# Optimization experiments

Measured on AMD Instinct MI355X. Metric: run time of the kernel, lower is better.

The kernel has to match this reference:

```python
import jax, jax.numpy as jnp
import numpy as np

N_NODES = 50000
N_EDGES = 800000
IN_FEATS = 256
HIDDEN = 128
OUT_FEATS = 64


def setup_inputs() -> dict:
    key = jax.random.key(0)
    k1, k2, k3, k4, k5 = jax.random.split(key, 5)
    x = jax.random.normal(k1, (N_NODES, IN_FEATS), dtype=jnp.float32)
    src = jax.random.randint(k2, (N_EDGES,), 0, N_NODES, dtype=jnp.int64)
    dst = jax.random.randint(k3, (N_EDGES,), 0, N_NODES, dtype=jnp.int64)
    # Glorot-ish init for linear weights (DGL GraphConv uses xavier_uniform)
    W1 = jax.random.normal(k4, (IN_FEATS, HIDDEN), dtype=jnp.float32) / np.sqrt(IN_FEATS)
    W2 = jax.random.normal(k5, (HIDDEN, OUT_FEATS), dtype=jnp.float32) / np.sqrt(HIDDEN)
    b1 = jnp.zeros((HIDDEN,), dtype=jnp.float32)
    b2 = jnp.zeros((OUT_FEATS,), dtype=jnp.float32)
    return {"x": x, "src": src, "dst": dst, "W1": W1, "b1": b1, "W2": W2, "b2": b2}


def _norms(src, dst, n_nodes):
    ones = jnp.ones(src.shape[0], dtype=jnp.float32)
    deg_out = jax.ops.segment_sum(ones, src, num_segments=n_nodes)
    deg_in = jax.ops.segment_sum(ones, dst, num_segments=n_nodes)
    # DGL clamps zero degrees to 1 to avoid inf
    norm_src = jnp.power(jnp.clip(deg_out, 1.0, None), -0.5)  # [N]
    norm_dst = jnp.power(jnp.clip(deg_in, 1.0, None), -0.5)   # [N]
    return norm_src, norm_dst


def _gcn_layer(h, W, b, src, dst, norm_src, norm_dst, n_nodes):
    # norm='both': D_dst^{-1/2} A D_src^{-1/2} (h W) + b
    # multiply by W first (in_feats >= out_feats -> cheaper aggregation)
    m = (h * norm_src[:, None]) @ W            # [N, out]
    agg = jax.ops.segment_sum(m[src], dst, num_segments=n_nodes)  # [N, out]
    return agg * norm_dst[:, None] + b


def reference(x, src, dst, W1, b1, W2, b2):
    n = x.shape[0]
    norm_src, norm_dst = _norms(src, dst, n)
    h = _gcn_layer(x, W1, b1, src, dst, norm_src, norm_dst, n)
    h = jax.nn.relu(h)
    h = _gcn_layer(h, W2, b2, src, dst, norm_src, norm_dst, n)
    return h
```

## Files before the change

### kernel.cpp

```cpp
#include <hip/hip_runtime.h>

#define N_NODES 50000
#define N_EDGES 800000
#define IN_FEATS 256
#define HIDDEN 128
#define OUT_FEATS 64

#define NB 8192
#define NRANGE 7
#define NBT (NRANGE * NB)
#define NCHUNK 64
#define EPC 12500

typedef _Float16 f16;
typedef _Float16 f16x2 __attribute__((ext_vector_type(2)));
typedef _Float16 f16x8 __attribute__((ext_vector_type(8)));
typedef float f32x4 __attribute__((ext_vector_type(4)));

__global__ __launch_bounds__(256) void hist_kernel(
    const int* __restrict__ src, const int* __restrict__ dst,
    int* __restrict__ hist_src, int* __restrict__ hist_dst) {
  __shared__ int ls[NB];
  __shared__ int ld2[NB];
  const int r = blockIdx.x % NRANGE;
  const int c = blockIdx.x / NRANGE;
  const int lo = r * NB;
  for (int i = threadIdx.x; i < NB; i += 256) {
    ls[i] = 0;
    ld2[i] = 0;
  }
  __syncthreads();
  const int4* s4 = (const int4*)(src + c * EPC);
  const int4* d4 = (const int4*)(dst + c * EPC);
  for (int i = threadIdx.x; i < EPC / 4; i += 256) {
    int4 s = s4[i];
    int4 d = d4[i];
    unsigned b;
    b = (unsigned)(s.x - lo); if (b < NB) atomicAdd(&ls[b], 1);
    b = (unsigned)(s.y - lo); if (b < NB) atomicAdd(&ls[b], 1);
    b = (unsigned)(s.z - lo); if (b < NB) atomicAdd(&ls[b], 1);
    b = (unsigned)(s.w - lo); if (b < NB) atomicAdd(&ls[b], 1);
    b = (unsigned)(d.x - lo); if (b < NB) atomicAdd(&ld2[b], 1);
    b = (unsigned)(d.y - lo); if (b < NB) atomicAdd(&ld2[b], 1);
    b = (unsigned)(d.z - lo); if (b < NB) atomicAdd(&ld2[b], 1);
    b = (unsigned)(d.w - lo); if (b < NB) atomicAdd(&ld2[b], 1);
  }
  __syncthreads();
  int* hs = hist_src + (long)c * NBT + lo;
  int* hd = hist_dst + (long)c * NBT + lo;
  for (int i = threadIdx.x; i < NB; i += 256) {
    hs[i] = ls[i];
    hd[i] = ld2[i];
  }
}

__global__ __launch_bounds__(256) void reduce_kernel(
    const int* __restrict__ hist_src, int* __restrict__ hist_dst,
    int* __restrict__ deg_in, float* __restrict__ norm_src,
    float* __restrict__ norm_dst) {
  int n = blockIdx.x * 256 + threadIdx.x;
  if (n >= N_NODES) return;
  int so = 0;
#pragma unroll 8
  for (int c = 0; c < NCHUNK; ++c) so += hist_src[(long)c * NBT + n];
  norm_src[n] = rsqrtf((float)max(so, 1));
  int run = 0;
#pragma unroll 8
  for (int c = 0; c < NCHUNK; ++c) {
    int t = hist_dst[(long)c * NBT + n];
    hist_dst[(long)c * NBT + n] = run;
    run += t;
  }
  deg_in[n] = run;
  norm_dst[n] = rsqrtf((float)max(run, 1));
}

__global__ __launch_bounds__(256) void scan1(const int* __restrict__ deg,
                                             int* __restrict__ partial) {
  __shared__ int sd[256];
  int i = blockIdx.x * 256 + threadIdx.x;
  sd[threadIdx.x] = (i < N_NODES) ? deg[i] : 0;
  __syncthreads();
  for (int s = 128; s > 0; s >>= 1) {
    if (threadIdx.x < s) sd[threadIdx.x] += sd[threadIdx.x + s];
    __syncthreads();
  }
  if (threadIdx.x == 0) partial[blockIdx.x] = sd[0];
}

__global__ __launch_bounds__(256) void scan2(int* __restrict__ partial,
                                             int nb) {
  __shared__ int sd[256];
  int v = (threadIdx.x < nb) ? partial[threadIdx.x] : 0;
  sd[threadIdx.x] = v;
  __syncthreads();
  for (int off = 1; off < 256; off <<= 1) {
    int t = sd[threadIdx.x] +
            ((threadIdx.x >= off) ? sd[threadIdx.x - off] : 0);
    __syncthreads();
    sd[threadIdx.x] = t;
    __syncthreads();
  }
  if (threadIdx.x < nb) partial[threadIdx.x] = sd[threadIdx.x] - v;
}

__global__ __launch_bounds__(256) void scan3(const int* __restrict__ deg,
                                             const int* __restrict__ partial,
                                             int* __restrict__ rowptr) {
  __shared__ int sd[256];
  int i = blockIdx.x * 256 + threadIdx.x;
  int v = (i < N_NODES) ? deg[i] : 0;
  sd[threadIdx.x] = v;
  __syncthreads();
  for (int off = 1; off < 256; off <<= 1) {
    int t = sd[threadIdx.x] +
            ((threadIdx.x >= off) ? sd[threadIdx.x - off] : 0);
    __syncthreads();
    sd[threadIdx.x] = t;
    __syncthreads();
  }
  if (i < N_NODES) rowptr[i] = partial[blockIdx.x] + sd[threadIdx.x] - v;
  if (blockIdx.x == 0 && threadIdx.x == 0) rowptr[N_NODES] = N_EDGES;
}

__global__ __launch_bounds__(256) void fill_csr(
    const int* __restrict__ src, const int* __restrict__ dst,
    const int* __restrict__ rowptr, const int* __restrict__ pref,
    int* __restrict__ col) {
  __shared__ int cur[NB];
  const int r = blockIdx.x % NRANGE;
  const int c = blockIdx.x / NRANGE;
  const int lo = r * NB;
  for (int i = threadIdx.x; i < NB; i += 256) {
    int n = lo + i;
    cur[i] = (n < N_NODES) ? rowptr[n] + pref[(long)c * NBT + n] : 0;
  }
  __syncthreads();
  const int4* s4 = (const int4*)(src + c * EPC);
  const int4* d4 = (const int4*)(dst + c * EPC);
  for (int i = threadIdx.x; i < EPC / 4; i += 256) {
    int4 s = s4[i];
    int4 d = d4[i];
    unsigned b;
    b = (unsigned)(d.x - lo);
    if (b < NB) col[atomicAdd(&cur[b], 1)] = s.x;
    b = (unsigned)(d.y - lo);
    if (b < NB) col[atomicAdd(&cur[b], 1)] = s.y;
    b = (unsigned)(d.z - lo);
    if (b < NB) col[atomicAdd(&cur[b], 1)] = s.z;
    b = (unsigned)(d.w - lo);
    if (b < NB) col[atomicAdd(&cur[b], 1)] = s.w;
  }
}

__global__ __launch_bounds__(256) void wtrans(const float* __restrict__ W1,
                                              const float* __restrict__ W2,
                                              f16* __restrict__ W1T,
                                              f16* __restrict__ W2T) {
  int i = blockIdx.x * 256 + threadIdx.x;
  if (i < 128 * 256) {
    int n = i >> 8, k = i & 255;
    W1T[i] = (f16)W1[k * 128 + n];
  } else if (i < 128 * 256 + 64 * 128) {
    int j = i - 128 * 256;
    int n = j >> 7, k = j & 127;
    W2T[j] = (f16)W2[k * 64 + n];
  }
}

template <int K, int NC, bool FP32IN>
__global__ __launch_bounds__(256) void gemm_mfma(
    const void* __restrict__ Xv, const f16* __restrict__ WT,
    const float* __restrict__ ns, f16* __restrict__ Mout) {
  constexpr int KI = K / 32;
  constexpr int NT = NC / 16;
  const int wave = threadIdx.x >> 6;
  const int lane = threadIdx.x & 63;
  const int m = lane & 15;
  const int q = lane >> 4;
  const int wrow0 = blockIdx.x * 128 + wave * 32;

  const int ra0 = min(wrow0 + m, N_NODES - 1);
  const int ra1 = min(wrow0 + 16 + m, N_NODES - 1);
  const float s0 = FP32IN ? ns[ra0] : 0.f;
  const float s1 = FP32IN ? ns[ra1] : 0.f;

  f32x4 acc[2][NT];
#pragma unroll
  for (int ab = 0; ab < 2; ++ab)
#pragma unroll
    for (int t = 0; t < NT; ++t) acc[ab][t] = (f32x4){0.f, 0.f, 0.f, 0.f};

#pragma unroll
  for (int ki = 0; ki < KI; ++ki) {
    const int kbase = ki * 32 + q * 8;
    f16x8 a0, a1;
    if (FP32IN) {
      const float* X = (const float*)Xv;
      const float* p0 = X + (long)ra0 * K + kbase;
      const float* p1 = X + (long)ra1 * K + kbase;
      float4 u0 = *(const float4*)p0;
      float4 u1 = *(const float4*)(p0 + 4);
      float4 w0 = *(const float4*)p1;
      float4 w1 = *(const float4*)(p1 + 4);
      a0[0] = (f16)(u0.x * s0); a0[1] = (f16)(u0.y * s0);
      a0[2] = (f16)(u0.z * s0); a0[3] = (f16)(u0.w * s0);
      a0[4] = (f16)(u1.x * s0); a0[5] = (f16)(u1.y * s0);
      a0[6] = (f16)(u1.z * s0); a0[7] = (f16)(u1.w * s0);
      a1[0] = (f16)(w0.x * s1); a1[1] = (f16)(w0.y * s1);
      a1[2] = (f16)(w0.z * s1); a1[3] = (f16)(w0.w * s1);
      a1[4] = (f16)(w1.x * s1); a1[5] = (f16)(w1.y * s1);
      a1[6] = (f16)(w1.z * s1); a1[7] = (f16)(w1.w * s1);
    } else {
      const f16* X = (const f16*)Xv;
      a0 = *(const f16x8*)(X + (long)ra0 * K + kbase);
      a1 = *(const f16x8*)(X + (long)ra1 * K + kbase);
    }
#pragma unroll
    for (int t = 0; t < NT; ++t) {
      f16x8 b = *(const f16x8*)(WT + (long)(t * 16 + m) * K + kbase);
      acc[0][t] =
          __builtin_amdgcn_mfma_f32_16x16x32_f16(a0, b, acc[0][t], 0, 0, 0);
      acc[1][t] =
          __builtin_amdgcn_mfma_f32_16x16x32_f16(a1, b, acc[1][t], 0, 0, 0);
    }
  }

#pragma unroll
  for (int ab = 0; ab < 2; ++ab)
#pragma unroll
    for (int r = 0; r < 4; ++r) {
      int row = wrow0 + ab * 16 + q * 4 + r;
      if (row < N_NODES) {
#pragma unroll
        for (int t = 0; t < NT; ++t)
          Mout[(long)row * NC + t * 16 + m] = (f16)acc[ab][t][r];
      }
    }
}

__global__ __launch_bounds__(256) void gather1_kernel(
    const f16* __restrict__ M, const int* __restrict__ rowptr,
    const int* __restrict__ col, const float* __restrict__ nd,
    const float* __restrict__ ns, const float* __restrict__ b,
    f16* __restrict__ out) {
  const int wave = threadIdx.x >> 6;
  const int lane = threadIdx.x & 63;
  const int n = blockIdx.x * 4 + wave;
  if (n >= N_NODES) return;
  const int beg = rowptr[n];
  const int end = rowptr[n + 1];

  float ax = 0.f, ay = 0.f;
  int i = beg;
  for (; i + 3 < end; i += 4) {
    int s0 = col[i], s1 = col[i + 1], s2 = col[i + 2], s3 = col[i + 3];
    f16x2 v0 = *(const f16x2*)(M + (long)s0 * HIDDEN + lane * 2);
    f16x2 v1 = *(const f16x2*)(M + (long)s1 * HIDDEN + lane * 2);
    f16x2 v2 = *(const f16x2*)(M + (long)s2 * HIDDEN + lane * 2);
    f16x2 v3 = *(const f16x2*)(M + (long)s3 * HIDDEN + lane * 2);
    ax += (float)v0[0] + (float)v1[0] + (float)v2[0] + (float)v3[0];
    ay += (float)v0[1] + (float)v1[1] + (float)v2[1] + (float)v3[1];
  }
  for (; i < end; ++i) {
    f16x2 v = *(const f16x2*)(M + (long)col[i] * HIDDEN + lane * 2);
    ax += (float)v[0];
    ay += (float)v[1];
  }
  float s = nd[n];
  float sn = ns[n];
  float ox = fmaxf(ax * s + b[lane * 2], 0.f) * sn;
  float oy = fmaxf(ay * s + b[lane * 2 + 1], 0.f) * sn;
  f16x2 o;
  o[0] = (f16)ox;
  o[1] = (f16)oy;
  *(f16x2*)(out + (long)n * HIDDEN + lane * 2) = o;
}

__global__ __launch_bounds__(256) void gather2_kernel(
    const f16* __restrict__ M, const int* __restrict__ rowptr,
    const int* __restrict__ col, const float* __restrict__ nd,
    const float* __restrict__ b, float* __restrict__ out) {
  const int wave = threadIdx.x >> 6;
  const int lane = threadIdx.x & 63;
  const int n = blockIdx.x * 4 + wave;
  if (n >= N_NODES) return;
  const int beg = rowptr[n];
  const int end = rowptr[n + 1];

  float acc = 0.f;
  int i = beg;
  for (; i + 3 < end; i += 4) {
    int s0 = col[i], s1 = col[i + 1], s2 = col[i + 2], s3 = col[i + 3];
    acc += (float)M[(long)s0 * OUT_FEATS + lane] +
           (float)M[(long)s1 * OUT_FEATS + lane] +
           (float)M[(long)s2 * OUT_FEATS + lane] +
           (float)M[(long)s3 * OUT_FEATS + lane];
  }
  for (; i < end; ++i) acc += (float)M[(long)col[i] * OUT_FEATS + lane];
  out[(long)n * OUT_FEATS + lane] = acc * nd[n] + b[lane];
}

extern "C" void kernel_launch(void* const* d_in, const int* in_sizes, int n_in,
                              void* d_out, int out_size, void* d_ws,
                              size_t ws_size, hipStream_t stream) {
  const float* x = (const float*)d_in[0];
  const int* src = (const int*)d_in[1];
  const int* dst = (const int*)d_in[2];
  const float* W1 = (const float*)d_in[3];
  const float* b1 = (const float*)d_in[4];
  const float* W2 = (const float*)d_in[5];
  const float* b2 = (const float*)d_in[6];
  float* out = (float*)d_out;

  int* wi = (int*)d_ws;
  int* partial = wi;
  int* rowptr = wi + 256;
  int* deg_in = wi + 50260;
  int* col = wi + 100260;
  float* wf = (float*)d_ws + 900260;
  float* norm_src = wf;
  float* norm_dst = wf + 50000;
  f16* fh = (f16*)(wf + 100000);
  f16* W1T = fh;
  f16* W2T = fh + 128 * 256;
  f16* m1 = fh + 128 * 256 + 64 * 128;
  f16* h1p = m1 + (long)50048 * 128;
  f16* m2 = h1p + (long)50048 * 128;

  int* hist_src = (int*)m1;
  int* hist_dst = hist_src + (long)NCHUNK * NBT;

  const int nb_nodes = (N_NODES + 255) / 256;

  hist_kernel<<<NRANGE * NCHUNK, 256, 0, stream>>>(src, dst, hist_src,
                                                   hist_dst);
  reduce_kernel<<<nb_nodes, 256, 0, stream>>>(hist_src, hist_dst, deg_in,
                                              norm_src, norm_dst);
  scan1<<<nb_nodes, 256, 0, stream>>>(deg_in, partial);
  scan2<<<1, 256, 0, stream>>>(partial, nb_nodes);
  scan3<<<nb_nodes, 256, 0, stream>>>(deg_in, partial, rowptr);
  fill_csr<<<NRANGE * NCHUNK, 256, 0, stream>>>(src, dst, rowptr, hist_dst,
                                                col);
  wtrans<<<(128 * 256 + 64 * 128 + 255) / 256, 256, 0, stream>>>(W1, W2, W1T,
                                                                 W2T);

  gemm_mfma<IN_FEATS, HIDDEN, true>
      <<<(N_NODES + 127) / 128, 256, 0, stream>>>(x, W1T, norm_src, m1);
  gather1_kernel<<<(N_NODES + 3) / 4, 256, 0, stream>>>(m1, rowptr, col,
                                                        norm_dst, norm_src, b1,
                                                        h1p);

  gemm_mfma<HIDDEN, OUT_FEATS, false>
      <<<(N_NODES + 127) / 128, 256, 0, stream>>>(h1p, W2T, norm_src, m2);
  gather2_kernel<<<(N_NODES + 3) / 4, 256, 0, stream>>>(m2, rowptr, col,
                                                        norm_dst, b2, out);
}
```

Before: 265.1 us.

## Vectorize CSR gathers with multi-edge lane groups and fuse scan1 into reduce

Both gather kernels now split each wave into lane groups that each load a full 16-byte f16x8 slice of a neighbor row, so several edges are processed in parallel per wave. Partial sums are combined with xor shuffles before one group writes the output. Separately, the block-sum step of the prefix scan is folded into reduce_kernel, which removes one launch and one re-read of deg_in. The cost is extra shuffle reductions and more registers per lane in the gathers.

```diff
diff --git a/kernel.cpp b/kernel.cpp
--- a/kernel.cpp
+++ b/kernel.cpp
@@ -57,29 +57,25 @@
 __global__ __launch_bounds__(256) void reduce_kernel(
     const int* __restrict__ hist_src, int* __restrict__ hist_dst,
     int* __restrict__ deg_in, float* __restrict__ norm_src,
-    float* __restrict__ norm_dst) {
+    float* __restrict__ norm_dst, int* __restrict__ partial) {
   int n = blockIdx.x * 256 + threadIdx.x;
-  if (n >= N_NODES) return;
-  int so = 0;
+  int run = 0;
+  if (n < N_NODES) {
+    int so = 0;
 #pragma unroll 8
-  for (int c = 0; c < NCHUNK; ++c) so += hist_src[(long)c * NBT + n];
-  norm_src[n] = rsqrtf((float)max(so, 1));
-  int run = 0;
+    for (int c = 0; c < NCHUNK; ++c) so += hist_src[(long)c * NBT + n];
+    norm_src[n] = rsqrtf((float)max(so, 1));
 #pragma unroll 8
-  for (int c = 0; c < NCHUNK; ++c) {
-    int t = hist_dst[(long)c * NBT + n];
-    hist_dst[(long)c * NBT + n] = run;
-    run += t;
-  }
-  deg_in[n] = run;
-  norm_dst[n] = rsqrtf((float)max(run, 1));
-}
-
-__global__ __launch_bounds__(256) void scan1(const int* __restrict__ deg,
-                                             int* __restrict__ partial) {
+    for (int c = 0; c < NCHUNK; ++c) {
+      int t = hist_dst[(long)c * NBT + n];
+      hist_dst[(long)c * NBT + n] = run;
+      run += t;
+    }
+    deg_in[n] = run;
+    norm_dst[n] = rsqrtf((float)max(run, 1));
+  }
   __shared__ int sd[256];
-  int i = blockIdx.x * 256 + threadIdx.x;
-  sd[threadIdx.x] = (i < N_NODES) ? deg[i] : 0;
+  sd[threadIdx.x] = run;
   __syncthreads();
   for (int s = 128; s > 0; s >>= 1) {
     if (threadIdx.x < s) sd[threadIdx.x] += sd[threadIdx.x + s];
@@ -244,61 +240,116 @@
     const int* __restrict__ col, const float* __restrict__ nd,
     const float* __restrict__ ns, const float* __restrict__ b,
     f16* __restrict__ out) {
+  constexpr int LPR = 16;
+  constexpr int EPW = 64 / LPR;
   const int wave = threadIdx.x >> 6;
   const int lane = threadIdx.x & 63;
+  const int g = lane / LPR;
+  const int t = lane % LPR;
   const int n = blockIdx.x * 4 + wave;
   if (n >= N_NODES) return;
   const int beg = rowptr[n];
   const int end = rowptr[n + 1];
 
-  float ax = 0.f, ay = 0.f;
-  int i = beg;
-  for (; i + 3 < end; i += 4) {
-    int s0 = col[i], s1 = col[i + 1], s2 = col[i + 2], s3 = col[i + 3];
-    f16x2 v0 = *(const f16x2*)(M + (long)s0 * HIDDEN + lane * 2);
-    f16x2 v1 = *(const f16x2*)(M + (long)s1 * HIDDEN + lane * 2);
-    f16x2 v2 = *(const f16x2*)(M + (long)s2 * HIDDEN + lane * 2);
-    f16x2 v3 = *(const f16x2*)(M + (long)s3 * HIDDEN + lane * 2);
-    ax += (float)v0[0] + (float)v1[0] + (float)v2[0] + (float)v3[0];
-    ay += (float)v0[1] + (float)v1[1] + (float)v2[1] + (float)v3[1];
-  }
-  for (; i < end; ++i) {
-    f16x2 v = *(const f16x2*)(M + (long)col[i] * HIDDEN + lane * 2);
-    ax += (float)v[0];
-    ay += (float)v[1];
-  }
-  float s = nd[n];
-  float sn = ns[n];
-  float ox = fmaxf(ax * s + b[lane * 2], 0.f) * sn;
-  float oy = fmaxf(ay * s + b[lane * 2 + 1], 0.f) * sn;
-  f16x2 o;
-  o[0] = (f16)ox;
-  o[1] = (f16)oy;
-  *(f16x2*)(out + (long)n * HIDDEN + lane * 2) = o;
+  float acc[8];
+#pragma unroll
+  for (int j = 0; j < 8; ++j) acc[j] = 0.f;
+
+  int i = beg + g;
+  for (; i + EPW < end; i += 2 * EPW) {
+    int s0 = col[i];
+    int s1 = col[i + EPW];
+    f16x8 v0 = *(const f16x8*)(M + (long)s0 * HIDDEN + t * 8);
+    f16x8 v1 = *(const f16x8*)(M + (long)s1 * HIDDEN + t * 8);
+#pragma unroll
+    for (int j = 0; j < 8; ++j) acc[j] += (float)v0[j] + (float)v1[j];
+  }
+  if (i < end) {
+    int s0 = col[i];
+    f16x8 v0 = *(const f16x8*)(M + (long)s0 * HIDDEN + t * 8);
+#pragma unroll
+    for (int j = 0; j < 8; ++j) acc[j] += (float)v0[j];
+  }
+
+#pragma unroll
+  for (int m2 = LPR; m2 < 64; m2 <<= 1)
+#pragma unroll
+    for (int j = 0; j < 8; ++j) acc[j] += __shfl_xor(acc[j], m2, 64);
+
+  if (g == 0) {
+    float s = nd[n];
+    float sn = ns[n];
+    float4 bb0 = *(const float4*)(b + t * 8);
+    float4 bb1 = *(const float4*)(b + t * 8 + 4);
+    f16x8 o;
+    o[0] = (f16)(fmaxf(acc[0] * s + bb0.x, 0.f) * sn);
+    o[1] = (f16)(fmaxf(acc[1] * s + bb0.y, 0.f) * sn);
+    o[2] = (f16)(fmaxf(acc[2] * s + bb0.z, 0.f) * sn);
+    o[3] = (f16)(fmaxf(acc[3] * s + bb0.w, 0.f) * sn);
+    o[4] = (f16)(fmaxf(acc[4] * s + bb1.x, 0.f) * sn);
+    o[5] = (f16)(fmaxf(acc[5] * s + bb1.y, 0.f) * sn);
+    o[6] = (f16)(fmaxf(acc[6] * s + bb1.z, 0.f) * sn);
+    o[7] = (f16)(fmaxf(acc[7] * s + bb1.w, 0.f) * sn);
+    *(f16x8*)(out + (long)n * HIDDEN + t * 8) = o;
+  }
 }
 
 __global__ __launch_bounds__(256) void gather2_kernel(
     const f16* __restrict__ M, const int* __restrict__ rowptr,
     const int* __restrict__ col, const float* __restrict__ nd,
     const float* __restrict__ b, float* __restrict__ out) {
+  constexpr int LPR = 8;
+  constexpr int EPW = 64 / LPR;
   const int wave = threadIdx.x >> 6;
   const int lane = threadIdx.x & 63;
+  const int g = lane / LPR;
+  const int t = lane % LPR;
   const int n = blockIdx.x * 4 + wave;
   if (n >= N_NODES) return;
   const int beg = rowptr[n];
   const int end = rowptr[n + 1];
 
-  float acc = 0.f;
-  int i = beg;
-  for (; i + 3 < end; i += 4) {
-    int s0 = col[i], s1 = col[i + 1], s2 = col[i + 2], s3 = col[i + 3];
-    acc += (float)M[(long)s0 * OUT_FEATS + lane] +
-           (float)M[(long)s1 * OUT_FEATS + lane] +
-           (float)M[(long)s2 * OUT_FEATS + lane] +
-           (float)M[(long)s3 * OUT_FEATS + lane];
-  }
-  for (; i < end; ++i) acc += (float)M[(long)col[i] * OUT_FEATS + lane];
-  out[(long)n * OUT_FEATS + lane] = acc * nd[n] + b[lane];
+  float acc[8];
+#pragma unroll
+  for (int j = 0; j < 8; ++j) acc[j] = 0.f;
+
+  int i = beg + g;
+  for (; i + EPW < end; i += 2 * EPW) {
+    int s0 = col[i];
+    int s1 = col[i + EPW];
+    f16x8 v0 = *(const f16x8*)(M + (long)s0 * OUT_FEATS + t * 8);
+    f16x8 v1 = *(const f16x8*)(M + (long)s1 * OUT_FEATS + t * 8);
+#pragma unroll
+    for (int j = 0; j < 8; ++j) acc[j] += (float)v0[j] + (float)v1[j];
+  }
+  if (i < end) {
+    int s0 = col[i];
+    f16x8 v0 = *(const f16x8*)(M + (long)s0 * OUT_FEATS + t * 8);
+#pragma unroll
+    for (int j = 0; j < 8; ++j) acc[j] += (float)v0[j];
+  }
+
+#pragma unroll
+  for (int m2 = LPR; m2 < 64; m2 <<= 1)
+#pragma unroll
+    for (int j = 0; j < 8; ++j) acc[j] += __shfl_xor(acc[j], m2, 64);
+
+  if (g == 0) {
+    float s = nd[n];
+    float4 bb0 = *(const float4*)(b + t * 8);
+    float4 bb1 = *(const float4*)(b + t * 8 + 4);
+    float4 o0, o1;
+    o0.x = acc[0] * s + bb0.x;
+    o0.y = acc[1] * s + bb0.y;
+    o0.z = acc[2] * s + bb0.z;
+    o0.w = acc[3] * s + bb0.w;
+    o1.x = acc[4] * s + bb1.x;
+    o1.y = acc[5] * s + bb1.y;
+    o1.z = acc[6] * s + bb1.z;
+    o1.w = acc[7] * s + bb1.w;
+    *(float4*)(out + (long)n * OUT_FEATS + t * 8) = o0;
+    *(float4*)(out + (long)n * OUT_FEATS + t * 8 + 4) = o1;
+  }
 }
 
 extern "C" void kernel_launch(void* const* d_in, const int* in_sizes, int n_in,
@@ -336,8 +387,7 @@
   hist_kernel<<<NRANGE * NCHUNK, 256, 0, stream>>>(src, dst, hist_src,
                                                    hist_dst);
   reduce_kernel<<<nb_nodes, 256, 0, stream>>>(hist_src, hist_dst, deg_in,
-                                              norm_src, norm_dst);
-  scan1<<<nb_nodes, 256, 0, stream>>>(deg_in, partial);
+                                              norm_src, norm_dst, partial);
   scan2<<<1, 256, 0, stream>>>(partial, nb_nodes);
   scan3<<<nb_nodes, 256, 0, stream>>>(deg_in, partial, rowptr);
   fill_csr<<<NRANGE * NCHUNK, 256, 0, stream>>>(src, dst, rowptr, hist_dst,
```

Result: faster. 249.6 us (-5.8%).
